# Optimization experiments

Measured on AMD Instinct MI355X. Metric: run time of the kernel, lower is better.

The kernel has to match this reference:

```python
import jax, jax.numpy as jnp
import numpy as np

N = 4096   # num ROIs across the batch (sgdet: ~8 images x 512 proposals)
H = 256    # rl_input_size == rl_hidden_size (hard-coded in __init__)
C = 151    # Visual Genome object classes incl. background


def setup_inputs() -> dict:
    key = jax.random.key(0)
    ks = jax.random.split(key, 7)
    prepro_feat = jax.random.normal(ks[0], (N, H), jnp.float32)
    d = jax.random.uniform(ks[1], (N, C), jnp.float32)
    obj_distributions = d / d.sum(-1, keepdims=True)  # softmax-like class probs
    co_occour = jax.random.uniform(ks[2], (C, C), jnp.float32)
    W_sub = jax.random.normal(ks[3], (H, H), jnp.float32) / np.sqrt(H)
    b_sub = jnp.zeros((H,), jnp.float32)
    W_obj = jax.random.normal(ks[4], (H, H), jnp.float32) / np.sqrt(H)
    b_obj = jnp.zeros((H,), jnp.float32)
    w_scores = jax.random.normal(ks[5], (3 * H + 3,), jnp.float32) / np.sqrt(3 * H + 3)
    b_scores = jnp.zeros((), jnp.float32)
    return dict(prepro_feat=prepro_feat, obj_distributions=obj_distributions,
                co_occour=co_occour, W_sub=W_sub, b_sub=b_sub,
                W_obj=W_obj, b_obj=b_obj, w_scores=w_scores, b_scores=b_scores)


def reference(prepro_feat, obj_distributions, co_occour, W_sub, b_sub,
              W_obj, b_obj, w_scores, b_scores):
    n = prepro_feat.shape[0]
    h = W_sub.shape[1]
    # label_scores = co_occour.sum(1)
    label_scores = co_occour.sum(1)                                   # [C]
    # rl_sub/rl_obj Linear + ReLU. In the torch expand, pair (i,j) uses sub[j], obj[i].
    sub = jax.nn.relu(prepro_feat @ W_sub + b_sub)                    # [N,H]
    obj = jax.nn.relu(prepro_feat @ W_obj + b_obj)                    # [N,H]
    # pair_score[i,j] = sum_{a,b} dist[j,a] * dist[i,b] * co[a,b]  (detached)
    pair_score = jax.lax.stop_gradient(
        jnp.einsum('ja,ab,ib->ij', obj_distributions, co_occour, obj_distributions))  # [N,N]
    s = jax.lax.stop_gradient(obj_distributions @ label_scores)       # [N]
    sub_score = s[None, :]   # varies along j
    obj_score = s[:, None]   # varies along i
    # rl_scores Linear over concat(sub*obj, sub, obj, pair, sub_score, obj_score),
    # decomposed exactly into its blocks (avoids the [N,N,3H+3] intermediate).
    w_mul, w_s, w_o = w_scores[:h], w_scores[h:2 * h], w_scores[2 * h:3 * h]
    w_ps, w_ss, w_os = w_scores[3 * h], w_scores[3 * h + 1], w_scores[3 * h + 2]
    pair_out = ((obj * w_mul) @ sub.T                                 # [i,j] = sum_h obj[i,h]*sub[j,h]*w_mul[h]
                + (sub @ w_s)[None, :]
                + (obj @ w_o)[:, None]
                + w_ps * pair_score + w_ss * sub_score + w_os * obj_score
                + b_scores)                                           # [N,N]
    pair_gates = jax.nn.sigmoid(pair_out).reshape(-1, 1)              # [N*N, 1]
    return pair_gates
```

## Files before the change

kernel.cpp:

```cpp
#include <hip/hip_runtime.h>
#include <hip/hip_bf16.h>
#include <math.h>

#define N_DIM 4096
#define H_DIM 256
#define C_DIM 151
#define KP    448
#define KT    160

typedef unsigned short ushort_t;
typedef __attribute__((ext_vector_type(8))) short bf16x8;
typedef __attribute__((ext_vector_type(4))) float f32x4;

#define WSB_PPACK  0
#define WSB_WT     2097152
#define WSB_DPACK  2359296
#define WSB_COT    3670016
#define WSB_PART   3731456
#define WSB_SPART  3993600
#define WSB_APACK  4091904
#define WSB_BPACK  7761920

#define GLL(src, dst) __builtin_amdgcn_global_load_lds( \
    (const __attribute__((address_space(1))) void*)(src), \
    (__attribute__((address_space(3))) void*)(dst), 16, 0, 0)

__global__ __launch_bounds__(256) void k_cvt(
    const float* __restrict__ P, const float* __restrict__ Ws,
    const float* __restrict__ Wo, const float* __restrict__ D,
    const float* __restrict__ co, const float* __restrict__ wsc,
    __hip_bfloat16* __restrict__ Pp, __hip_bfloat16* __restrict__ Wt,
    __hip_bfloat16* __restrict__ Dpack, __hip_bfloat16* __restrict__ coT,
    __hip_bfloat16* __restrict__ Apack) {
    __shared__ float shbuf[64 * C_DIM];
    const int t = threadIdx.x;
    const int bid = blockIdx.x;
    if (bid < 512) {
        int idx = (bid * 256 + t) * 8;
        float4 a = *(const float4*)(P + idx);
        float4 b = *(const float4*)(P + idx + 4);
        __hip_bfloat16 h[8];
        h[0] = __float2bfloat16(a.x); h[1] = __float2bfloat16(a.y);
        h[2] = __float2bfloat16(a.z); h[3] = __float2bfloat16(a.w);
        h[4] = __float2bfloat16(b.x); h[5] = __float2bfloat16(b.y);
        h[6] = __float2bfloat16(b.z); h[7] = __float2bfloat16(b.w);
        *(bf16x8*)&Pp[idx] = *(bf16x8*)h;
    } else if (bid < 544) {
        const int b  = bid - 512;
        const int k0 = (b & 3) * 64;
        const int h0 = ((b >> 2) & 3) * 64;
        const int z  = b >> 4;
        const float* W = z ? Wo : Ws;
        #pragma unroll
        for (int q = 0; q < 4; ++q) {
            int r = (t >> 4) + q * 16;
            int c = (t & 15) * 4;
            float4 f = *(const float4*)&W[(size_t)(k0 + r) * H_DIM + h0 + c];
            shbuf[r * 65 + c] = f.x; shbuf[r * 65 + c + 1] = f.y;
            shbuf[r * 65 + c + 2] = f.z; shbuf[r * 65 + c + 3] = f.w;
        }
        __syncthreads();
        #pragma unroll
        for (int q = 0; q < 2; ++q) {
            int idx = t + q * 256;
            int h   = idx >> 3;
            int kc  = idx & 7;
            __hip_bfloat16 u[8];
            #pragma unroll
            for (int j = 0; j < 8; ++j)
                u[j] = __float2bfloat16(shbuf[(kc * 8 + j) * 65 + h]);
            *(bf16x8*)&Wt[((size_t)z * H_DIM + h0 + h) * H_DIM + k0 + kc * 8] = *(bf16x8*)u;
        }
    } else if (bid < 608) {
        const int b  = bid - 544;
        const int i0 = b * 64;
        for (int idx = t; idx < 64 * C_DIM; idx += 256)
            shbuf[idx] = D[(size_t)i0 * C_DIM + idx];
        __syncthreads();
        const float wps = wsc[768];
        for (int o = t; o < 64 * (KT / 8); o += 256) {
            int r = o / (KT / 8), ch = o % (KT / 8);
            __hip_bfloat16 u[8];
            #pragma unroll
            for (int j = 0; j < 8; ++j) {
                int k = ch * 8 + j;
                u[j] = __float2bfloat16(k < C_DIM ? shbuf[r * C_DIM + k] : 0.f);
            }
            *(bf16x8*)&Dpack[(size_t)(i0 + r) * KT + ch * 8] = *(bf16x8*)u;
        }
        for (int o = t; o < 64 * 24; o += 256) {
            int r = o / 24, ch = o % 24;
            __hip_bfloat16 u[8];
            #pragma unroll
            for (int j = 0; j < 8; ++j) {
                int c = ch * 8 + j;
                u[j] = __float2bfloat16(c < C_DIM ? wps * shbuf[r * C_DIM + c] : 0.f);
            }
            *(bf16x8*)&Apack[(size_t)(i0 + r) * KP + H_DIM + ch * 8] = *(bf16x8*)u;
        }
    } else {
        const int q  = bid - 608;
        const int a0 = (q % 3) * 64;
        const int c0 = (q / 3) * 64;
        for (int o = t; o < 64 * 64; o += 256) {
            int r = o >> 6, c = o & 63;
            float v = 0.f;
            if (a0 + r < C_DIM && c0 + c < C_DIM)
                v = co[(size_t)(a0 + r) * C_DIM + c0 + c];
            shbuf[r * 65 + c] = v;
        }
        __syncthreads();
        const int nch = (a0 == 128) ? 4 : 8;
        for (int o = t; o < 64 * 8; o += 256) {
            int cl = o >> 3, ch = o & 7;
            if (ch < nch) {
                __hip_bfloat16 u[8];
                #pragma unroll
                for (int j = 0; j < 8; ++j)
                    u[j] = __float2bfloat16(shbuf[(ch * 8 + j) * 65 + cl]);
                *(bf16x8*)&coT[(size_t)(c0 + cl) * KT + a0 + ch * 8] = *(bf16x8*)u;
            }
        }
    }
}

__global__ __launch_bounds__(256) void k_mid(
    const ushort_t* __restrict__ Pp, const ushort_t* __restrict__ Wt,
    const ushort_t* __restrict__ Dpack, const ushort_t* __restrict__ coT,
    const float* __restrict__ bsub, const float* __restrict__ bobj,
    const float* __restrict__ wsc,
    __hip_bfloat16* __restrict__ Apack, __hip_bfloat16* __restrict__ Bpack,
    float* __restrict__ part, float* __restrict__ spart) {
    __shared__ ushort_t As[128 * 256];
    __shared__ ushort_t Bs[64 * 256];

    const int t = threadIdx.x;
    const int w = t >> 6, l = t & 63;
    const int wr = w >> 1, wc = w & 1;
    const int lr = l & 15, g = l >> 4;
    const int bid = blockIdx.x;

    if (bid < 256) {
        const int hblk = bid & 3;
        const int i0   = ((bid >> 2) & 31) * 128;
        const int z    = bid >> 7;
        const int j0   = hblk * 64;
        const float* bias = z ? bobj : bsub;
        const ushort_t* Wz = Wt + (size_t)z * H_DIM * H_DIM;

        #pragma unroll
        for (int r_ = 0; r_ < 16; ++r_) {
            int idx = t + r_ * 256, row = idx >> 5, cl = idx & 31;
            int cs = cl ^ (row & 7);
            GLL(Pp + (size_t)(i0 + row) * H_DIM + cs * 8, &As[idx * 8]);
        }
        #pragma unroll
        for (int r_ = 0; r_ < 8; ++r_) {
            int idx = t + r_ * 256, row = idx >> 5, cl = idx & 31;
            int cs = cl ^ (row & 7);
            GLL(Wz + (size_t)(j0 + row) * H_DIM + cs * 8, &Bs[idx * 8]);
        }
        __syncthreads();

        f32x4 acc[4][2];
        #pragma unroll
        for (int m = 0; m < 4; ++m)
            #pragma unroll
            for (int n = 0; n < 2; ++n) acc[m][n] = f32x4{0.f, 0.f, 0.f, 0.f};

        #pragma unroll
        for (int ks2 = 0; ks2 < 8; ++ks2) {
            bf16x8 a[4], b[2];
            int c = ks2 * 4 + g;
            #pragma unroll
            for (int m = 0; m < 4; ++m) {
                int Rl = wr * 64 + m * 16 + lr;
                int cl = c ^ (Rl & 7);
                a[m] = *(const bf16x8*)&As[(Rl * 32 + cl) * 8];
            }
            #pragma unroll
            for (int n = 0; n < 2; ++n) {
                int Rl = wc * 32 + n * 16 + lr;
                int cl = c ^ (Rl & 7);
                b[n] = *(const bf16x8*)&Bs[(Rl * 32 + cl) * 8];
            }
            #pragma unroll
            for (int m = 0; m < 4; ++m)
                #pragma unroll
                for (int n = 0; n < 2; ++n)
                    acc[m][n] = __builtin_amdgcn_mfma_f32_16x16x32_bf16(
                        a[m], b[n], acc[m][n], 0, 0, 0);
        }

        int hn[2]; float bb[2], wse[2], wmu[2];
        #pragma unroll
        for (int n = 0; n < 2; ++n) {
            hn[n]  = j0 + wc * 32 + n * 16 + lr;
            bb[n]  = bias[hn[n]];
            wse[n] = wsc[(z ? 512 : 256) + hn[n]];
            wmu[n] = wsc[hn[n]];
        }
        float* partq = part + (size_t)(z * 8 + hblk * 2 + wc) * N_DIM;
        #pragma unroll
        for (int m = 0; m < 4; ++m) {
            float p[4] = {0.f, 0.f, 0.f, 0.f};
            #pragma unroll
            for (int n = 0; n < 2; ++n)
                #pragma unroll
                for (int r = 0; r < 4; ++r) {
                    float v = acc[m][n][r] + bb[n];
                    v = v > 0.f ? v : 0.f;
                    int i = i0 + wr * 64 + m * 16 + g * 4 + r;
                    if (z) Apack[(size_t)i * KP + hn[n]] = __float2bfloat16(v * wmu[n]);
                    else   Bpack[(size_t)i * KP + hn[n]] = __float2bfloat16(v);
                    p[r] += v * wse[n];
                }
            #pragma unroll
            for (int r = 0; r < 4; ++r) {
                p[r] += __shfl_xor(p[r], 1);
                p[r] += __shfl_xor(p[r], 2);
                p[r] += __shfl_xor(p[r], 4);
                p[r] += __shfl_xor(p[r], 8);
            }
            if (lr == 0)
                #pragma unroll
                for (int r = 0; r < 4; ++r)
                    partq[i0 + wr * 64 + m * 16 + g * 4 + r] = p[r];
        }
    } else {
        const int q  = bid - 256;
        const int j0 = (q % 3) * 64;
        const int i0 = (q / 3) * 64;

        bf16x8 a[2][5], b[2][5];
        #pragma unroll
        for (int m = 0; m < 2; ++m) {
            const ushort_t* ap = Dpack + (size_t)(i0 + wr * 32 + m * 16 + lr) * KT + g * 8;
            #pragma unroll
            for (int ks = 0; ks < 5; ++ks) a[m][ks] = *(const bf16x8*)(ap + ks * 32);
        }
        #pragma unroll
        for (int n = 0; n < 2; ++n) {
            const ushort_t* bp = coT + (size_t)(j0 + wc * 32 + n * 16 + lr) * KT + g * 8;
            #pragma unroll
            for (int ks = 0; ks < 5; ++ks) b[n][ks] = *(const bf16x8*)(bp + ks * 32);
        }

        f32x4 acc[2][2];
        #pragma unroll
        for (int m = 0; m < 2; ++m)
            #pragma unroll
            for (int n = 0; n < 2; ++n) acc[m][n] = f32x4{0.f, 0.f, 0.f, 0.f};
        #pragma unroll
        for (int ks = 0; ks < 5; ++ks)
            #pragma unroll
            for (int m = 0; m < 2; ++m)
                #pragma unroll
                for (int n = 0; n < 2; ++n)
                    acc[m][n] = __builtin_amdgcn_mfma_f32_16x16x32_bf16(
                        a[m][ks], b[n][ks], acc[m][n], 0, 0, 0);

        float* sp = spart + (size_t)((q % 3) * 2 + wc) * N_DIM;
        #pragma unroll
        for (int m = 0; m < 2; ++m) {
            float p[4] = {0.f, 0.f, 0.f, 0.f};
            #pragma unroll
            for (int n = 0; n < 2; ++n) {
                int col = j0 + wc * 32 + n * 16 + lr;
                #pragma unroll
                for (int r = 0; r < 4; ++r) {
                    int i = i0 + wr * 32 + m * 16 + g * 4 + r;
                    float v = acc[m][n][r];
                    Bpack[(size_t)i * KP + H_DIM + col] = __float2bfloat16(v);
                    p[r] += v;
                }
            }
            #pragma unroll
            for (int r = 0; r < 4; ++r) {
                p[r] += __shfl_xor(p[r], 1);
                p[r] += __shfl_xor(p[r], 2);
                p[r] += __shfl_xor(p[r], 4);
                p[r] += __shfl_xor(p[r], 8);
            }
            if (lr == 0)
                #pragma unroll
                for (int r = 0; r < 4; ++r)
                    sp[i0 + wr * 32 + m * 16 + g * 4 + r] = p[r];
        }
    }
}

__global__ __launch_bounds__(512) void k_main(
    const ushort_t* __restrict__ Apack, const ushort_t* __restrict__ Bpack,
    const float* __restrict__ part, const float* __restrict__ spart,
    const float* __restrict__ wsc, const float* __restrict__ bsc,
    float* __restrict__ out) {
    __shared__ ushort_t pa[2][256 * 64];
    __shared__ ushort_t pb[2][128 * 64];
    __shared__ float rbS[256], cbS[128];

    const int t = threadIdx.x;
    const int w = t >> 6, l = t & 63;
    const int wm = w >> 1, wn = w & 1;
    const int lr = l & 15, g = l >> 4;
    const int bid = blockIdx.x;
    const int wgid = (bid & 7) * 64 + (bid >> 3);
    const int i0 = (wgid >> 5) * 256;
    const int j0 = (wgid & 31) * 128;

#define K_STAGE(buf, ks) do {                                                   \
    _Pragma("unroll")                                                           \
    for (int r_ = 0; r_ < 4; ++r_) {                                            \
        int idx_ = t + r_ * 512, row_ = idx_ >> 3, cl_ = idx_ & 7;              \
        int cs_ = cl_ ^ (row_ & 7);                                             \
        GLL(Apack + (size_t)(i0+row_)*KP + (ks)*64 + cs_*8, &pa[buf][idx_*8]);  \
    }                                                                           \
    _Pragma("unroll")                                                           \
    for (int r_ = 0; r_ < 2; ++r_) {                                            \
        int idx_ = t + r_ * 512, row_ = idx_ >> 3, cl_ = idx_ & 7;              \
        int cs_ = cl_ ^ (row_ & 7);                                             \
        GLL(Bpack + (size_t)(j0+row_)*KP + (ks)*64 + cs_*8, &pb[buf][idx_*8]);  \
    }                                                                           \
} while (0)

    K_STAGE(0, 0);
    if (t < 256) {
        int i = i0 + t; float r = 0.f, si = 0.f;
        #pragma unroll
        for (int q = 8; q < 16; ++q) r += part[(size_t)q * N_DIM + i];
        #pragma unroll
        for (int q = 0; q < 6; ++q) si += spart[(size_t)q * N_DIM + i];
        rbS[t] = r + wsc[770] * si;
    } else if (t < 384) {
        int j = j0 + (t - 256); float c = 0.f, sj = 0.f;
        #pragma unroll
        for (int q = 0; q < 8; ++q) c += part[(size_t)q * N_DIM + j];
        #pragma unroll
        for (int q = 0; q < 6; ++q) sj += spart[(size_t)q * N_DIM + j];
        cbS[t - 256] = c + wsc[769] * sj + bsc[0];
    }
    __syncthreads();

    f32x4 acc[4][4];
    #pragma unroll
    for (int m = 0; m < 4; ++m)
        #pragma unroll
        for (int n = 0; n < 4; ++n) acc[m][n] = f32x4{0.f, 0.f, 0.f, 0.f};

    for (int ks = 0; ks < 7; ++ks) {
        const int cur = ks & 1;
        if (ks < 6) K_STAGE(cur ^ 1, ks + 1);
        #pragma unroll
        for (int ks2 = 0; ks2 < 2; ++ks2) {
            bf16x8 a[4], b[4];
            int c = ks2 * 4 + g;
            #pragma unroll
            for (int m = 0; m < 4; ++m) {
                int Rl = wm * 64 + m * 16 + lr;
                int cl = c ^ (Rl & 7);
                a[m] = *(const bf16x8*)&pa[cur][(Rl * 8 + cl) * 8];
            }
            #pragma unroll
            for (int n = 0; n < 4; ++n) {
                int Rl = wn * 64 + n * 16 + lr;
                int cl = c ^ (Rl & 7);
                b[n] = *(const bf16x8*)&pb[cur][(Rl * 8 + cl) * 8];
            }
            #pragma unroll
            for (int m = 0; m < 4; ++m)
                #pragma unroll
                for (int n = 0; n < 4; ++n)
                    acc[m][n] = __builtin_amdgcn_mfma_f32_16x16x32_bf16(
                        a[m], b[n], acc[m][n], 0, 0, 0);
        }
        __syncthreads();
    }
#undef K_STAGE

    float cbv[4];
    #pragma unroll
    for (int n = 0; n < 4; ++n) cbv[n] = cbS[wn * 64 + n * 16 + lr];
    float* OutS = (float*)pa;
    #pragma unroll
    for (int m = 0; m < 4; ++m) {
        #pragma unroll
        for (int n = 0; n < 4; ++n) {
            #pragma unroll
            for (int r = 0; r < 4; ++r) {
                float rb = rbS[wm * 64 + m * 16 + g * 4 + r];
                float v  = acc[m][n][r] + rb + cbv[n];
                float e  = __expf(-v);
                OutS[(wm * 16 + g * 4 + r) * 132 + wn * 64 + n * 16 + lr] =
                    __builtin_amdgcn_rcpf(1.0f + e);
            }
        }
        __syncthreads();
        {
            int rl = t >> 3, c8 = t & 7;
            int gr = i0 + (rl >> 4) * 64 + m * 16 + (rl & 15);
            float* op = out + (size_t)gr * N_DIM + j0;
            const float* rp = OutS + rl * 132;
            #pragma unroll
            for (int k = 0; k < 4; ++k) {
                float4 v4 = *(const float4*)(rp + (c8 + 8 * k) * 4);
                *(float4*)(op + (c8 + 8 * k) * 4) = v4;
            }
        }
        __syncthreads();
    }
}

extern "C" void kernel_launch(void* const* d_in, const int* in_sizes, int n_in,
                              void* d_out, int out_size, void* d_ws, size_t ws_size,
                              hipStream_t stream) {
    const float* prepro = (const float*)d_in[0];
    const float* D      = (const float*)d_in[1];
    const float* co     = (const float*)d_in[2];
    const float* Wsub   = (const float*)d_in[3];
    const float* bsub   = (const float*)d_in[4];
    const float* Wobj   = (const float*)d_in[5];
    const float* bobj   = (const float*)d_in[6];
    const float* wsc    = (const float*)d_in[7];
    const float* bsc    = (const float*)d_in[8];
    float* out = (float*)d_out;

    char* ws = (char*)d_ws;
    __hip_bfloat16* Ppack = (__hip_bfloat16*)(ws + WSB_PPACK);
    __hip_bfloat16* Wt    = (__hip_bfloat16*)(ws + WSB_WT);
    __hip_bfloat16* Dpack = (__hip_bfloat16*)(ws + WSB_DPACK);
    __hip_bfloat16* coT   = (__hip_bfloat16*)(ws + WSB_COT);
    float* part  = (float*)(ws + WSB_PART);
    float* spart = (float*)(ws + WSB_SPART);
    __hip_bfloat16* Apack = (__hip_bfloat16*)(ws + WSB_APACK);
    __hip_bfloat16* Bpack = (__hip_bfloat16*)(ws + WSB_BPACK);

    k_cvt<<<617, 256, 0, stream>>>(prepro, Wsub, Wobj, D, co, wsc,
                                   Ppack, Wt, Dpack, coT, Apack);
    k_mid<<<448, 256, 0, stream>>>(
        (const ushort_t*)Ppack, (const ushort_t*)Wt,
        (const ushort_t*)Dpack, (const ushort_t*)coT,
        bsub, bobj, wsc, Apack, Bpack, part, spart);
    k_main<<<512, 512, 0, stream>>>(
        (const ushort_t*)Apack, (const ushort_t*)Bpack, part, spart, wsc, bsc, out);
}
```

Before: 54.15 us.

## Load MFMA fragments directly from global and shrink main-kernel tile to 128x128

The main pair-score GEMM kernel no longer stages A/B tiles through LDS with global_load_lds double buffering. Each wave now loads its bf16 fragments straight from global memory into registers, using a two-stage register ping-pong. The tile shrinks from 256x128 with 512 threads to 128x128 with 256 threads, doubling the grid to 1024 blocks. This drops LDS traffic and per-K-step barriers and frees LDS for more resident blocks, but operands are no longer shared through LDS, which raises global/L2 load traffic. The epilogue is also restructured to write two 64-row halves using raw barriers.

```diff
diff --git a/kernel.cpp b/kernel.cpp
--- a/kernel.cpp
+++ b/kernel.cpp
@@ -290,123 +290,121 @@
     }
 }
 
-__global__ __launch_bounds__(512) void k_main(
+__global__ __launch_bounds__(256) void k_main(
     const ushort_t* __restrict__ Apack, const ushort_t* __restrict__ Bpack,
     const float* __restrict__ part, const float* __restrict__ spart,
     const float* __restrict__ wsc, const float* __restrict__ bsc,
     float* __restrict__ out) {
-    __shared__ ushort_t pa[2][256 * 64];
-    __shared__ ushort_t pb[2][128 * 64];
-    __shared__ float rbS[256], cbS[128];
+    __shared__ float OutS[64 * 132];
+    __shared__ float rbS[128], cbS[128];
 
     const int t = threadIdx.x;
     const int w = t >> 6, l = t & 63;
-    const int wm = w >> 1, wn = w & 1;
+    const int wr = w >> 1, wc = w & 1;
     const int lr = l & 15, g = l >> 4;
     const int bid = blockIdx.x;
-    const int wgid = (bid & 7) * 64 + (bid >> 3);
-    const int i0 = (wgid >> 5) * 256;
-    const int j0 = (wgid & 31) * 128;
-
-#define K_STAGE(buf, ks) do {                                                   \
-    _Pragma("unroll")                                                           \
-    for (int r_ = 0; r_ < 4; ++r_) {                                            \
-        int idx_ = t + r_ * 512, row_ = idx_ >> 3, cl_ = idx_ & 7;              \
-        int cs_ = cl_ ^ (row_ & 7);                                             \
-        GLL(Apack + (size_t)(i0+row_)*KP + (ks)*64 + cs_*8, &pa[buf][idx_*8]);  \
-    }                                                                           \
-    _Pragma("unroll")                                                           \
-    for (int r_ = 0; r_ < 2; ++r_) {                                            \
-        int idx_ = t + r_ * 512, row_ = idx_ >> 3, cl_ = idx_ & 7;              \
-        int cs_ = cl_ ^ (row_ & 7);                                             \
-        GLL(Bpack + (size_t)(j0+row_)*KP + (ks)*64 + cs_*8, &pb[buf][idx_*8]);  \
-    }                                                                           \
-} while (0)
-
-    K_STAGE(0, 0);
-    if (t < 256) {
+    const int swz = (bid & 7) * 128 + (bid >> 3);
+    const int i0 = (swz >> 5) * 128;
+    const int j0 = (swz & 31) * 128;
+
+    if (t < 128) {
         int i = i0 + t; float r = 0.f, si = 0.f;
         #pragma unroll
         for (int q = 8; q < 16; ++q) r += part[(size_t)q * N_DIM + i];
         #pragma unroll
         for (int q = 0; q < 6; ++q) si += spart[(size_t)q * N_DIM + i];
         rbS[t] = r + wsc[770] * si;
-    } else if (t < 384) {
-        int j = j0 + (t - 256); float c = 0.f, sj = 0.f;
+    } else {
+        int j = j0 + (t - 128); float c = 0.f, sj = 0.f;
         #pragma unroll
         for (int q = 0; q < 8; ++q) c += part[(size_t)q * N_DIM + j];
         #pragma unroll
         for (int q = 0; q < 6; ++q) sj += spart[(size_t)q * N_DIM + j];
-        cbS[t - 256] = c + wsc[769] * sj + bsc[0];
+        cbS[t - 128] = c + wsc[769] * sj + bsc[0];
     }
     __syncthreads();
 
+    const ushort_t* pa[4];
+    const ushort_t* pb[4];
+    #pragma unroll
+    for (int m = 0; m < 4; ++m)
+        pa[m] = Apack + (size_t)(i0 + wr * 64 + m * 16 + lr) * KP + g * 8;
+    #pragma unroll
+    for (int n = 0; n < 4; ++n)
+        pb[n] = Bpack + (size_t)(j0 + wc * 64 + n * 16 + lr) * KP + g * 8;
+
     f32x4 acc[4][4];
     #pragma unroll
     for (int m = 0; m < 4; ++m)
         #pragma unroll
         for (int n = 0; n < 4; ++n) acc[m][n] = f32x4{0.f, 0.f, 0.f, 0.f};
 
-    for (int ks = 0; ks < 7; ++ks) {
-        const int cur = ks & 1;
-        if (ks < 6) K_STAGE(cur ^ 1, ks + 1);
-        #pragma unroll
-        for (int ks2 = 0; ks2 < 2; ++ks2) {
-            bf16x8 a[4], b[4];
-            int c = ks2 * 4 + g;
-            #pragma unroll
-            for (int m = 0; m < 4; ++m) {
-                int Rl = wm * 64 + m * 16 + lr;
-                int cl = c ^ (Rl & 7);
-                a[m] = *(const bf16x8*)&pa[cur][(Rl * 8 + cl) * 8];
-            }
-            #pragma unroll
-            for (int n = 0; n < 4; ++n) {
-                int Rl = wn * 64 + n * 16 + lr;
-                int cl = c ^ (Rl & 7);
-                b[n] = *(const bf16x8*)&pb[cur][(Rl * 8 + cl) * 8];
-            }
+#define LOADF(A_, B_, ks) do {                                                  \
+    _Pragma("unroll")                                                           \
+    for (int m_ = 0; m_ < 4; ++m_) A_[m_] = *(const bf16x8*)(pa[m_] + (ks)*32); \
+    _Pragma("unroll")                                                           \
+    for (int n_ = 0; n_ < 4; ++n_) B_[n_] = *(const bf16x8*)(pb[n_] + (ks)*32); \
+} while (0)
+
+#define MFMAS(A_, B_) do {                                                      \
+    _Pragma("unroll")                                                           \
+    for (int m_ = 0; m_ < 4; ++m_)                                              \
+        _Pragma("unroll")                                                       \
+        for (int n_ = 0; n_ < 4; ++n_)                                          \
+            acc[m_][n_] = __builtin_amdgcn_mfma_f32_16x16x32_bf16(              \
+                A_[m_], B_[n_], acc[m_][n_], 0, 0, 0);                          \
+} while (0)
+
+    bf16x8 a0[4], b0[4], a1[4], b1[4];
+    LOADF(a0, b0, 0);
+    #pragma unroll
+    for (int kk = 0; kk < 6; ++kk) {
+        LOADF(a1, b1, 2 * kk + 1);
+        MFMAS(a0, b0);
+        LOADF(a0, b0, 2 * kk + 2);
+        MFMAS(a1, b1);
+    }
+    LOADF(a1, b1, 13);
+    MFMAS(a0, b0);
+    MFMAS(a1, b1);
+#undef LOADF
+#undef MFMAS
+
+    float cbv[4];
+    #pragma unroll
+    for (int n = 0; n < 4; ++n) cbv[n] = cbS[wc * 64 + n * 16 + lr];
+
+    #pragma unroll
+    for (int mh = 0; mh < 2; ++mh) {
+        if (wr == mh) {
             #pragma unroll
             for (int m = 0; m < 4; ++m)
                 #pragma unroll
                 for (int n = 0; n < 4; ++n)
-                    acc[m][n] = __builtin_amdgcn_mfma_f32_16x16x32_bf16(
-                        a[m], b[n], acc[m][n], 0, 0, 0);
-        }
-        __syncthreads();
-    }
-#undef K_STAGE
-
-    float cbv[4];
-    #pragma unroll
-    for (int n = 0; n < 4; ++n) cbv[n] = cbS[wn * 64 + n * 16 + lr];
-    float* OutS = (float*)pa;
-    #pragma unroll
-    for (int m = 0; m < 4; ++m) {
-        #pragma unroll
-        for (int n = 0; n < 4; ++n) {
-            #pragma unroll
-            for (int r = 0; r < 4; ++r) {
-                float rb = rbS[wm * 64 + m * 16 + g * 4 + r];
-                float v  = acc[m][n][r] + rb + cbv[n];
-                float e  = __expf(-v);
-                OutS[(wm * 16 + g * 4 + r) * 132 + wn * 64 + n * 16 + lr] =
-                    __builtin_amdgcn_rcpf(1.0f + e);
-            }
-        }
-        __syncthreads();
+                    #pragma unroll
+                    for (int r = 0; r < 4; ++r) {
+                        int rl = m * 16 + g * 4 + r;
+                        float v = acc[m][n][r] + rbS[wr * 64 + rl] + cbv[n];
+                        float e = __expf(-v);
+                        OutS[rl * 132 + wc * 64 + n * 16 + lr] =
+                            __builtin_amdgcn_rcpf(1.0f + e);
+                    }
+        }
+        asm volatile("s_waitcnt lgkmcnt(0)" ::: "memory");
+        __builtin_amdgcn_s_barrier();
+        __builtin_amdgcn_sched_barrier(0);
         {
-            int rl = t >> 3, c8 = t & 7;
-            int gr = i0 + (rl >> 4) * 64 + m * 16 + (rl & 15);
-            float* op = out + (size_t)gr * N_DIM + j0;
-            const float* rp = OutS + rl * 132;
-            #pragma unroll
-            for (int k = 0; k < 4; ++k) {
-                float4 v4 = *(const float4*)(rp + (c8 + 8 * k) * 4);
-                *(float4*)(op + (c8 + 8 * k) * 4) = v4;
-            }
-        }
-        __syncthreads();
+            int row = t >> 2, seg = t & 3;
+            const float* rp = OutS + row * 132 + seg * 32;
+            float* op = out + (size_t)(i0 + mh * 64 + row) * N_DIM + j0 + seg * 32;
+            #pragma unroll
+            for (int k = 0; k < 8; ++k) {
+                float4 v4 = *(const float4*)(rp + k * 4);
+                *(float4*)(op + k * 4) = v4;
+            }
+        }
+        __builtin_amdgcn_s_barrier();
+        __builtin_amdgcn_sched_barrier(0);
     }
 }
 
@@ -440,6 +438,6 @@
         (const ushort_t*)Ppack, (const ushort_t*)Wt,
         (const ushort_t*)Dpack, (const ushort_t*)coT,
         bsub, bobj, wsc, Apack, Bpack, part, spart);
-    k_main<<<512, 512, 0, stream>>>(
+    k_main<<<1024, 256, 0, stream>>>(
         (const ushort_t*)Apack, (const ushort_t*)Bpack, part, spart, wsc, bsc, out);
 }
```

Result: slower. 99.11 us (+83.0%).

## Single-buffer LDS K-loop and stage epilogue by warp-row

Applied to the files above, without the earlier changes.

Replaces the double-buffered LDS staging with a single buffer, so each K step now computes, syncs, loads the next tile and syncs again. This removes the overlap between global loads and MFMA work in exchange for half the LDS footprint, which may allow more workgroups per CU. The epilogue is reorganised so only one warp-row writes its 64x128 slab to LDS per pass before a contiguous store, while the other warps idle at barriers.

```diff
diff --git a/kernel.cpp b/kernel.cpp
--- a/kernel.cpp
+++ b/kernel.cpp
@@ -295,35 +295,62 @@
     const float* __restrict__ part, const float* __restrict__ spart,
     const float* __restrict__ wsc, const float* __restrict__ bsc,
     float* __restrict__ out) {
-    __shared__ ushort_t pa[2][256 * 64];
-    __shared__ ushort_t pb[2][128 * 64];
+    __shared__ ushort_t pool[(256 + 128) * 64];
     __shared__ float rbS[256], cbS[128];
+    ushort_t* As = pool;
+    ushort_t* Bs = pool + 256 * 64;
 
     const int t = threadIdx.x;
     const int w = t >> 6, l = t & 63;
     const int wm = w >> 1, wn = w & 1;
     const int lr = l & 15, g = l >> 4;
     const int bid = blockIdx.x;
-    const int wgid = (bid & 7) * 64 + (bid >> 3);
-    const int i0 = (wgid >> 5) * 256;
-    const int j0 = (wgid & 31) * 128;
-
-#define K_STAGE(buf, ks) do {                                                   \
+    const int swz = (bid & 7) * 64 + (bid >> 3);
+    const int i0 = (swz >> 5) * 256;
+    const int j0 = (swz & 31) * 128;
+
+#define K_STAGE(ks) do {                                                        \
     _Pragma("unroll")                                                           \
     for (int r_ = 0; r_ < 4; ++r_) {                                            \
         int idx_ = t + r_ * 512, row_ = idx_ >> 3, cl_ = idx_ & 7;              \
         int cs_ = cl_ ^ (row_ & 7);                                             \
-        GLL(Apack + (size_t)(i0+row_)*KP + (ks)*64 + cs_*8, &pa[buf][idx_*8]);  \
+        GLL(Apack + (size_t)(i0+row_)*KP + (ks)*64 + cs_*8, &As[idx_*8]);       \
     }                                                                           \
     _Pragma("unroll")                                                           \
     for (int r_ = 0; r_ < 2; ++r_) {                                            \
         int idx_ = t + r_ * 512, row_ = idx_ >> 3, cl_ = idx_ & 7;              \
         int cs_ = cl_ ^ (row_ & 7);                                             \
-        GLL(Bpack + (size_t)(j0+row_)*KP + (ks)*64 + cs_*8, &pb[buf][idx_*8]);  \
+        GLL(Bpack + (size_t)(j0+row_)*KP + (ks)*64 + cs_*8, &Bs[idx_*8]);       \
     }                                                                           \
 } while (0)
 
-    K_STAGE(0, 0);
+#define K_COMPUTE() do {                                                        \
+    _Pragma("unroll")                                                           \
+    for (int ks2 = 0; ks2 < 2; ++ks2) {                                         \
+        bf16x8 a[4], b[4];                                                      \
+        int c = ks2 * 4 + g;                                                    \
+        _Pragma("unroll")                                                       \
+        for (int m_ = 0; m_ < 4; ++m_) {                                        \
+            int Rl = wm * 64 + m_ * 16 + lr;                                    \
+            int cl = c ^ (Rl & 7);                                              \
+            a[m_] = *(const bf16x8*)&As[(Rl * 8 + cl) * 8];                     \
+        }                                                                       \
+        _Pragma("unroll")                                                       \
+        for (int n_ = 0; n_ < 4; ++n_) {                                        \
+            int Rl = wn * 64 + n_ * 16 + lr;                                    \
+            int cl = c ^ (Rl & 7);                                              \
+            b[n_] = *(const bf16x8*)&Bs[(Rl * 8 + cl) * 8];                     \
+        }                                                                       \
+        _Pragma("unroll")                                                       \
+        for (int m_ = 0; m_ < 4; ++m_)                                          \
+            _Pragma("unroll")                                                   \
+            for (int n_ = 0; n_ < 4; ++n_)                                      \
+                acc[m_][n_] = __builtin_amdgcn_mfma_f32_16x16x32_bf16(          \
+                    a[m_], b[n_], acc[m_][n_], 0, 0, 0);                        \
+    }                                                                           \
+} while (0)
+
+    K_STAGE(0);
     if (t < 256) {
         int i = i0 + t; float r = 0.f, si = 0.f;
         #pragma unroll
@@ -347,63 +374,48 @@
         #pragma unroll
         for (int n = 0; n < 4; ++n) acc[m][n] = f32x4{0.f, 0.f, 0.f, 0.f};
 
+    #pragma unroll 1
     for (int ks = 0; ks < 7; ++ks) {
-        const int cur = ks & 1;
-        if (ks < 6) K_STAGE(cur ^ 1, ks + 1);
-        #pragma unroll
-        for (int ks2 = 0; ks2 < 2; ++ks2) {
-            bf16x8 a[4], b[4];
-            int c = ks2 * 4 + g;
-            #pragma unroll
-            for (int m = 0; m < 4; ++m) {
-                int Rl = wm * 64 + m * 16 + lr;
-                int cl = c ^ (Rl & 7);
-                a[m] = *(const bf16x8*)&pa[cur][(Rl * 8 + cl) * 8];
-            }
-            #pragma unroll
-            for (int n = 0; n < 4; ++n) {
-                int Rl = wn * 64 + n * 16 + lr;
-                int cl = c ^ (Rl & 7);
-                b[n] = *(const bf16x8*)&pb[cur][(Rl * 8 + cl) * 8];
-            }
-            #pragma unroll
-            for (int m = 0; m < 4; ++m)
-                #pragma unroll
-                for (int n = 0; n < 4; ++n)
-                    acc[m][n] = __builtin_amdgcn_mfma_f32_16x16x32_bf16(
-                        a[m], b[n], acc[m][n], 0, 0, 0);
-        }
-        __syncthreads();
+        K_COMPUTE();
+        if (ks < 6) {
+            __syncthreads();
+            K_STAGE(ks + 1);
+            __syncthreads();
+        }
     }
+    __syncthreads();
 #undef K_STAGE
+#undef K_COMPUTE
 
     float cbv[4];
     #pragma unroll
     for (int n = 0; n < 4; ++n) cbv[n] = cbS[wn * 64 + n * 16 + lr];
-    float* OutS = (float*)pa;
+    float* OutS = (float*)pool;
     #pragma unroll
-    for (int m = 0; m < 4; ++m) {
-        #pragma unroll
-        for (int n = 0; n < 4; ++n) {
-            #pragma unroll
-            for (int r = 0; r < 4; ++r) {
-                float rb = rbS[wm * 64 + m * 16 + g * 4 + r];
-                float v  = acc[m][n][r] + rb + cbv[n];
-                float e  = __expf(-v);
-                OutS[(wm * 16 + g * 4 + r) * 132 + wn * 64 + n * 16 + lr] =
-                    __builtin_amdgcn_rcpf(1.0f + e);
-            }
+    for (int mc = 0; mc < 4; ++mc) {
+        if (wm == mc) {
+            #pragma unroll
+            for (int m = 0; m < 4; ++m)
+                #pragma unroll
+                for (int n = 0; n < 4; ++n)
+                    #pragma unroll
+                    for (int r = 0; r < 4; ++r) {
+                        int rl = m * 16 + g * 4 + r;
+                        float v = acc[m][n][r] + rbS[mc * 64 + rl] + cbv[n];
+                        float e = __expf(-v);
+                        OutS[rl * 132 + wn * 64 + n * 16 + lr] =
+                            __builtin_amdgcn_rcpf(1.0f + e);
+                    }
         }
         __syncthreads();
         {
-            int rl = t >> 3, c8 = t & 7;
-            int gr = i0 + (rl >> 4) * 64 + m * 16 + (rl & 15);
-            float* op = out + (size_t)gr * N_DIM + j0;
-            const float* rp = OutS + rl * 132;
+            int row = t >> 3, seg = t & 7;
+            const float* rp = OutS + row * 132;
+            float* op = out + (size_t)(i0 + mc * 64 + row) * N_DIM + j0;
             #pragma unroll
             for (int k = 0; k < 4; ++k) {
-                float4 v4 = *(const float4*)(rp + (c8 + 8 * k) * 4);
-                *(float4*)(op + (c8 + 8 * k) * 4) = v4;
+                float4 v4 = *(const float4*)(rp + (seg + 8 * k) * 4);
+                *(float4*)(op + (seg + 8 * k) * 4) = v4;
             }
         }
         __syncthreads();
```

Measured after the change: 49.51 us. 8.6% less time.
